# Performance work log

Measured on AMD Instinct MI355X. Metric: run time of the kernel, lower is better.

Reference implementation:

```python
import jax, jax.numpy as jnp
import numpy as np

D_MODEL = 256
N_LAYERS = 8
NUM_CLASSES = 3
INPUT_DIM = 1
BATCH = 8
SEQ = 2048
EXIT_IDX = (1, 3, 5, 7)  # n_layers//4-1, n_layers//2-1, 3n//4-1, n-1
LN_EPS = 1e-5


def setup_inputs() -> dict:
    key = jax.random.key(0)
    ks = jax.random.split(key, 16)
    d, nl, nc = D_MODEL, N_LAYERS, NUM_CLASSES
    return {
        "x": jax.random.normal(ks[0], (BATCH, SEQ, INPUT_DIM), jnp.float32),
        "in_W": jax.random.normal(ks[1], (d, INPUT_DIM), jnp.float32) * 0.02,
        "in_b": jnp.zeros((d,), jnp.float32),
        "A_params": jax.random.normal(ks[2], (nl, d), jnp.float32) * 0.1,
        "B_params": jax.random.normal(ks[3], (nl, d), jnp.float32),
        "C_params": jax.random.normal(ks[4], (nl, d), jnp.float32),
        "D_params": jax.random.normal(ks[5], (nl, d), jnp.float32),
        "proj_W": jax.random.normal(ks[6], (nl, d, d), jnp.float32) * 0.02,
        "proj_b": jnp.zeros((nl, d), jnp.float32),
        "ln_g": jnp.ones((nl, d), jnp.float32),
        "ln_b": jnp.zeros((nl, d), jnp.float32),
        "head_W": jax.random.normal(ks[7], (4, nc, d), jnp.float32) * 0.02,
        "head_b": jnp.zeros((4, nc), jnp.float32),
    }


def _ssm_block(x, Ap, Bp, Cp, Dp, pW, pb, g, b):
    # x: [B, L, d]
    Bsz, L, d = x.shape
    A = jax.nn.sigmoid(Ap)                               # [d]
    t = jnp.arange(L, dtype=jnp.float32)
    K = (Cp[:, None] * (A[:, None] ** t[None, :]) * Bp[:, None])[:, None, :]  # [d,1,L]
    xt = jnp.swapaxes(x, 1, 2)                           # [B, d, L]
    # torch F.conv1d(pad=L-1, groups=d) then [..., :L] == left-pad-only cross-correlation
    out = jax.lax.conv_general_dilated(
        xt, K, window_strides=(1,), padding=[(L - 1, 0)], feature_group_count=d
    )                                                    # [B, d, L]
    out = out + Dp[None, :, None] * xt
    out = jnp.swapaxes(out, 1, 2)                        # [B, L, d]
    out = jax.nn.gelu(out, approximate=False) @ pW.T + pb
    y = x + out
    mu = jnp.mean(y, axis=-1, keepdims=True)
    var = jnp.var(y, axis=-1, keepdims=True)
    return (y - mu) / jnp.sqrt(var + LN_EPS) * g + b


def reference(x, in_W, in_b, A_params, B_params, C_params, D_params,
              proj_W, proj_b, ln_g, ln_b, head_W, head_b):
    h = x @ in_W.T + in_b                                # [B, L, d]
    logits = []
    head = 0
    for i in range(N_LAYERS):
        h = _ssm_block(h, A_params[i], B_params[i], C_params[i], D_params[i],
                       proj_W[i], proj_b[i], ln_g[i], ln_b[i])
        if i in EXIT_IDX:
            pooled = jnp.mean(h, axis=1)                 # [B, d]
            logits.append(pooled @ head_W[head].T + head_b[head])
            head += 1
    return jnp.stack(logits, axis=0)                     # [4, B, num_classes]
```

## Files before the change

### kernel.cpp

```cpp
#include <hip/hip_runtime.h>
#include <math.h>

#define DM 256
#define LSEQ 2048
#define BATCH 8
#define NLAYER 8
#define EMAX 192
#define LN_EPS 1e-5f
#define BM 32
#define BLKS 64
#define NPROD 7
#define TAILB 57
#define ROWS (BATCH * LSEQ)

#define HT_STRIDE 1040
#define AB_OFF   33280
#define AL_OFF   (AB_OFF + 16384)
#define RED_OFF  (AL_OFF + 16384)
#define SMEM_SZ  (RED_OFF + 1280)

typedef float f32x4 __attribute__((ext_vector_type(4)));
typedef short bf16x8 __attribute__((ext_vector_type(8)));
typedef unsigned short u16;
typedef unsigned short u16x4 __attribute__((ext_vector_type(4)));
typedef unsigned short u16x8 __attribute__((ext_vector_type(8)));

union V8 { u16x8 u; bf16x8 b; };

__device__ __forceinline__ float erf_fast(float x) {
    float ax = fabsf(x);
    float t = __builtin_amdgcn_rcpf(fmaf(0.3275911f, ax, 1.f));
    float p = fmaf(t, 1.061405429f, -1.453152027f);
    p = fmaf(t, p, 1.421413741f);
    p = fmaf(t, p, -0.284496736f);
    p = fmaf(t, p, 0.254829592f);
    p = p * t;
    float e = __expf(-ax * ax);
    float r = 1.f - p * e;
    return copysignf(r, x);
}

__device__ __forceinline__ float gelu_fast(float v) {
    return 0.5f * v * (1.f + erf_fast(v * 0.70710678118654752f));
}

__device__ __forceinline__ void split2(float g, u16& hi, u16& lo) {
    unsigned u = __float_as_uint(g);
    hi = (u16)(u >> 16);
    float fh = __uint_as_float(u & 0xFFFF0000u);
    float r = g - fh;
    unsigned v = __float_as_uint(r);
    v = v + 0x7FFFu + ((v >> 16) & 1u);
    lo = (u16)(v >> 16);
}

__global__ void k_prepW(const float* __restrict__ pW, u16* __restrict__ pWh,
                        u16* __restrict__ pWl) {
    int i = blockIdx.x * blockDim.x + threadIdx.x;
    int e = i * 8;
    int l = e >> 16;
    int r = e & 65535;
    int cg = r >> 12;
    int ks = (r >> 9) & 7;
    int lane = (r >> 3) & 63;
    int fq = lane >> 4, fr = lane & 15;
    int col = (cg >> 2) * 64 + (cg & 3) * 16 + fr;
    int k = ks * 32 + fq * 8;
    const float* src = pW + l * 65536 + col * 256 + k;
    float4 w0 = *(const float4*)src;
    float4 w1 = *(const float4*)(src + 4);
    float vv[8] = {w0.x, w0.y, w0.z, w0.w, w1.x, w1.y, w1.z, w1.w};
    u16 sh[8], sl[8];
#pragma unroll
    for (int j = 0; j < 8; ++j) split2(vv[j], sh[j], sl[j]);
    u16x8 vh = {sh[0], sh[1], sh[2], sh[3], sh[4], sh[5], sh[6], sh[7]};
    u16x8 vl = {sl[0], sl[1], sl[2], sl[3], sl[4], sl[5], sl[6], sl[7]};
    *(u16x8*)&pWh[e] = vh;
    *(u16x8*)&pWl[e] = vl;
}

__global__ void k_prep0(const float* __restrict__ x, const float* __restrict__ inW,
                        const float* __restrict__ inb, const float* __restrict__ Ap,
                        const float* __restrict__ Bp, const float* __restrict__ Cp,
                        float* __restrict__ P_all, float* __restrict__ logA_all,
                        float* __restrict__ CB_all, float* __restrict__ pooled,
                        int* __restrict__ flags) {
    int b = blockIdx.x;
    int c = threadIdx.x;
    float A0 = 1.f / (1.f + expf(-Ap[c]));
    float iw = inW[c], ib = inb[c];
    const float* xb = x + b * LSEQ;
    float pw = 1.f, acc = 0.f;
    for (int t = 0; t <= EMAX; ++t) {
        acc += (xb[t] * iw + ib) * pw;
        pw *= A0;
    }
    P_all[b * DM + c] = acc;
    for (int l = 1; l < NLAYER; ++l) P_all[l * BATCH * DM + b * DM + c] = 0.f;
    for (int e = 0; e < 4; ++e) pooled[e * BATCH * DM + b * DM + c] = 0.f;
    if (b == 0) {
        for (int l = 0; l < NLAYER; ++l) {
            float Al = 1.f / (1.f + expf(-Ap[l * DM + c]));
            logA_all[l * DM + c] = logf(Al);
            CB_all[l * DM + c]   = Bp[l * DM + c] * Cp[l * DM + c];
        }
        if (c < NLAYER * BATCH) flags[c] = 0;
    }
}

__global__ __launch_bounds__(256, 2) void k_fused(
    const float* __restrict__ x, const float* __restrict__ inW,
    const float* __restrict__ inb,
    const u16* __restrict__ pWh, const u16* __restrict__ pWl,
    const float* __restrict__ Dp_all, const float* __restrict__ pb_all,
    const float* __restrict__ lng_all, const float* __restrict__ lnb_all,
    const float* __restrict__ logA_all, const float* __restrict__ CB_all,
    float* __restrict__ P_all, float* __restrict__ pooled,
    int* __restrict__ flags)
{
    __shared__ __align__(16) char smem[SMEM_SZ];

    int tid  = threadIdx.x;
    int lane = tid & 63;
    int wn   = tid >> 6;
    int fr   = lane & 15;
    int fq   = lane >> 4;

    int b    = blockIdx.x >> 6;
    int blk  = blockIdx.x & 63;
    int brow = b * LSEQ + blk * BM;
    bool isTail = (blk >= TAILB);
    bool isProd = (blk < NPROD);

    int srow = tid >> 3;
    int gr_s = brow + srow;
    int t_s  = gr_s & (LSEQ - 1);
    int u_s  = (LSEQ - 1) - t_s;
    bool tail_s = (u_s <= EMAX);
    float uf = (float)u_s;
    float xv = x[gr_s];

    float hreg[2][4][4];
    float* Pbuf = (float*)(smem + RED_OFF);

    for (int l = 0; l < NLAYER; ++l) {
        const float* Dp  = Dp_all   + l * DM;
        const float* la  = logA_all + l * DM;
        const float* cbp = CB_all   + l * DM;

        if (isTail) {
            if (l >= 1 && tid == 0) {
                while (__hip_atomic_load(&flags[l * BATCH + b], __ATOMIC_ACQUIRE,
                                         __HIP_MEMORY_SCOPE_AGENT) < NPROD)
                    __builtin_amdgcn_s_sleep(2);
            }
            __syncthreads();
            if (tid < DM)
                Pbuf[tid] = __hip_atomic_load(
                    &P_all[(size_t)l * BATCH * DM + b * DM + tid],
                    __ATOMIC_RELAXED, __HIP_MEMORY_SCOPE_AGENT);
            __syncthreads();
        }

        const u16* bhp = pWh + (size_t)l * 65536 + wn * 16384 + lane * 8;
        const u16* blp = pWl + (size_t)l * 65536 + wn * 16384 + lane * 8;
        V8 bhd[2][4], bld[2][4];
#pragma unroll
        for (int n = 0; n < 4; ++n) {
            bhd[0][n].u = *(const u16x8*)&bhp[n * 4096];
            bld[0][n].u = *(const u16x8*)&blp[n * 4096];
        }

#pragma unroll
        for (int i = 0; i < 4; ++i) {
            int u  = (tid & 7) + 8 * i;
            int kk = u * 8;
            int hby = srow * HT_STRIDE + u * 32;
            float hv[8];
            if (l == 0) {
                float4 w0 = *(const float4*)&inW[kk], w1 = *(const float4*)&inW[kk + 4];
                float4 b0 = *(const float4*)&inb[kk], b1 = *(const float4*)&inb[kk + 4];
                hv[0] = fmaf(xv, w0.x, b0.x); hv[1] = fmaf(xv, w0.y, b0.y);
                hv[2] = fmaf(xv, w0.z, b0.z); hv[3] = fmaf(xv, w0.w, b0.w);
                hv[4] = fmaf(xv, w1.x, b1.x); hv[5] = fmaf(xv, w1.y, b1.y);
                hv[6] = fmaf(xv, w1.z, b1.z); hv[7] = fmaf(xv, w1.w, b1.w);
                float4 o0 = {hv[0], hv[1], hv[2], hv[3]};
                float4 o1 = {hv[4], hv[5], hv[6], hv[7]};
                *(float4*)(smem + hby) = o0;
                *(float4*)(smem + hby + 16) = o1;
            } else {
                float4 h0 = *(const float4*)(smem + hby);
                float4 h1 = *(const float4*)(smem + hby + 16);
                hv[0] = h0.x; hv[1] = h0.y; hv[2] = h0.z; hv[3] = h0.w;
                hv[4] = h1.x; hv[5] = h1.y; hv[6] = h1.z; hv[7] = h1.w;
            }
            float4 d0 = *(const float4*)&Dp[kk];
            float4 d1 = *(const float4*)&Dp[kk + 4];
            float vv[8];
            vv[0] = hv[0] * d0.x; vv[1] = hv[1] * d0.y;
            vv[2] = hv[2] * d0.z; vv[3] = hv[3] * d0.w;
            vv[4] = hv[4] * d1.x; vv[5] = hv[5] * d1.y;
            vv[6] = hv[6] * d1.z; vv[7] = hv[7] * d1.w;
            if (tail_s) {
                float4 la0 = *(const float4*)&la[kk],  la1 = *(const float4*)&la[kk + 4];
                float4 cb0 = *(const float4*)&cbp[kk], cb1 = *(const float4*)&cbp[kk + 4];
                float4 P0  = *(const float4*)&Pbuf[kk], P1 = *(const float4*)&Pbuf[kk + 4];
                vv[0] += cb0.x * __expf(uf * la0.x) * P0.x;
                vv[1] += cb0.y * __expf(uf * la0.y) * P0.y;
                vv[2] += cb0.z * __expf(uf * la0.z) * P0.z;
                vv[3] += cb0.w * __expf(uf * la0.w) * P0.w;
                vv[4] += cb1.x * __expf(uf * la1.x) * P1.x;
                vv[5] += cb1.y * __expf(uf * la1.y) * P1.y;
                vv[6] += cb1.z * __expf(uf * la1.z) * P1.z;
                vv[7] += cb1.w * __expf(uf * la1.w) * P1.w;
            }
            u16 sh[8], sl[8];
#pragma unroll
            for (int j = 0; j < 8; ++j) split2(gelu_fast(vv[j]), sh[j], sl[j]);
            u16x8 vh = {sh[0], sh[1], sh[2], sh[3], sh[4], sh[5], sh[6], sh[7]};
            u16x8 vl = {sl[0], sl[1], sl[2], sl[3], sl[4], sl[5], sl[6], sl[7]};
            int aby = srow * 512 + ((u ^ (srow & 7)) << 4);
            *(u16x8*)(smem + AB_OFF + aby) = vh;
            *(u16x8*)(smem + AL_OFF + aby) = vl;
        }
        __syncthreads();

        f32x4 acc[2][4];
#pragma unroll
        for (int m = 0; m < 2; ++m)
#pragma unroll
            for (int n = 0; n < 4; ++n) acc[m][n] = (f32x4){0.f, 0.f, 0.f, 0.f};

#pragma unroll
        for (int ks = 0; ks < 8; ++ks) {
            int cur = ks & 1, nxt = cur ^ 1;
            if (ks < 7) {
#pragma unroll
                for (int n = 0; n < 4; ++n) {
                    bhd[nxt][n].u = *(const u16x8*)&bhp[n * 4096 + (ks + 1) * 512];
                    bld[nxt][n].u = *(const u16x8*)&blp[n * 4096 + (ks + 1) * 512];
                }
            }
            V8 ah[2], al[2];
#pragma unroll
            for (int m = 0; m < 2; ++m) {
                int row = m * 16 + fr;
                int aby = row * 512 + (((ks * 4 + fq) ^ (row & 7)) << 4);
                ah[m].u = *(const u16x8*)(smem + AB_OFF + aby);
                al[m].u = *(const u16x8*)(smem + AL_OFF + aby);
            }
#pragma unroll
            for (int m = 0; m < 2; ++m)
#pragma unroll
                for (int n = 0; n < 4; ++n) {
                    acc[m][n] = __builtin_amdgcn_mfma_f32_16x16x32_bf16(ah[m].b, bhd[cur][n].b, acc[m][n], 0, 0, 0);
                    acc[m][n] = __builtin_amdgcn_mfma_f32_16x16x32_bf16(ah[m].b, bld[cur][n].b, acc[m][n], 0, 0, 0);
                    acc[m][n] = __builtin_amdgcn_mfma_f32_16x16x32_bf16(al[m].b, bhd[cur][n].b, acc[m][n], 0, 0, 0);
                }
        }

        if (l == 0) {
#pragma unroll
            for (int m = 0; m < 2; ++m)
#pragma unroll
                for (int n = 0; n < 4; ++n)
#pragma unroll
                    for (int r = 0; r < 4; ++r) {
                        int row = m * 16 + fq * 4 + r;
                        int col = wn * 64 + n * 16 + fr;
                        hreg[m][n][r] = *(const float*)(smem + row * HT_STRIDE + col * 4);
                    }
        }
        float pbv[4], lgv[4], lbv[4];
#pragma unroll
        for (int n = 0; n < 4; ++n) {
            int col = wn * 64 + n * 16 + fr;
            pbv[n] = pb_all[l * DM + col];
            lgv[n] = lng_all[l * DM + col];
            lbv[n] = lnb_all[l * DM + col];
        }
        float s[2][4], ss[2][4];
#pragma unroll
        for (int m = 0; m < 2; ++m)
#pragma unroll
            for (int r = 0; r < 4; ++r) {
                float sy = 0.f, sy2 = 0.f;
#pragma unroll
                for (int n = 0; n < 4; ++n) {
                    float y = hreg[m][n][r] + acc[m][n][r] + pbv[n];
                    acc[m][n][r] = y;
                    sy += y; sy2 += y * y;
                }
                s[m][r] = sy; ss[m][r] = sy2;
            }
#pragma unroll
        for (int m = 0; m < 2; ++m)
#pragma unroll
            for (int r = 0; r < 4; ++r)
#pragma unroll
                for (int msk = 1; msk < 16; msk <<= 1) {
                    s[m][r]  += __shfl_xor(s[m][r],  msk);
                    ss[m][r] += __shfl_xor(ss[m][r], msk);
                }
        if (fr == 0) {
#pragma unroll
            for (int m = 0; m < 2; ++m)
#pragma unroll
                for (int r = 0; r < 4; ++r) {
                    int row = m * 16 + fq * 4 + r;
                    *(float*)(smem + RED_OFF + (row * 10 + wn * 2)     * 4) = s[m][r];
                    *(float*)(smem + RED_OFF + (row * 10 + wn * 2 + 1) * 4) = ss[m][r];
                }
        }
        __syncthreads();

        float mean[2][4], rstd[2][4];
#pragma unroll
        for (int m = 0; m < 2; ++m)
#pragma unroll
            for (int r = 0; r < 4; ++r) {
                int row = m * 16 + fq * 4 + r;
                float st = 0.f, sst = 0.f;
#pragma unroll
                for (int w = 0; w < 4; ++w) {
                    st  += *(const float*)(smem + RED_OFF + (row * 10 + w * 2)     * 4);
                    sst += *(const float*)(smem + RED_OFF + (row * 10 + w * 2 + 1) * 4);
                }
                float mu = st * (1.f / 256.f);
                float var = sst * (1.f / 256.f) - mu * mu;
                mean[m][r] = mu;
                rstd[m][r] = rsqrtf(var + LN_EPS);
            }
        int slot = (l == 1) ? 0 : (l == 3) ? 1 : (l == 5) ? 2 : (l == 7) ? 3 : -1;
        bool prod = (l < NLAYER - 1) && isProd;
        float lanv[4];
        if (prod) {
            const float* lan = logA_all + (l + 1) * DM;
#pragma unroll
            for (int n = 0; n < 4; ++n) lanv[n] = lan[wn * 64 + n * 16 + fr];
        }
        float cs[4] = {0.f, 0.f, 0.f, 0.f};
        float pc[4] = {0.f, 0.f, 0.f, 0.f};
#pragma unroll
        for (int m = 0; m < 2; ++m)
#pragma unroll
            for (int r = 0; r < 4; ++r) {
                int row  = m * 16 + fq * 4 + r;
                int trow = blk * BM + row;
#pragma unroll
                for (int n = 0; n < 4; ++n) {
                    float o = (acc[m][n][r] - mean[m][r]) * rstd[m][r] * lgv[n] + lbv[n];
                    hreg[m][n][r] = o;
                    int col = wn * 64 + n * 16 + fr;
                    *(float*)(smem + row * HT_STRIDE + col * 4) = o;
                    if (slot >= 0) cs[n] += o;
                    if (prod && trow <= EMAX) pc[n] += o * __expf((float)trow * lanv[n]);
                }
            }
        if (slot >= 0) {
#pragma unroll
            for (int n = 0; n < 4; ++n) {
                cs[n] += __shfl_xor(cs[n], 16);
                cs[n] += __shfl_xor(cs[n], 32);
            }
            if (lane < 16) {
#pragma unroll
                for (int n = 0; n < 4; ++n)
                    atomicAdd(&pooled[slot * (BATCH * DM) + b * DM + wn * 64 + n * 16 + lane], cs[n]);
            }
        }
        if (prod) {
#pragma unroll
            for (int n = 0; n < 4; ++n) {
                pc[n] += __shfl_xor(pc[n], 16);
                pc[n] += __shfl_xor(pc[n], 32);
            }
            if (lane < 16) {
#pragma unroll
                for (int n = 0; n < 4; ++n)
                    atomicAdd(&P_all[(size_t)(l + 1) * BATCH * DM + b * DM + wn * 64 + n * 16 + lane], pc[n]);
            }
        }
        __syncthreads();
        if (prod && tid == 0)
            __hip_atomic_fetch_add(&flags[(l + 1) * BATCH + b], 1,
                                   __ATOMIC_RELEASE, __HIP_MEMORY_SCOPE_AGENT);
    }
}

__global__ void k_head(const float* __restrict__ pooled, const float* __restrict__ hW,
                       const float* __restrict__ hb, float* __restrict__ out) {
    int tid = threadIdx.x;
    if (tid >= 96) return;
    int e = tid / 24;
    int r = tid % 24;
    int b = r / 3;
    int n = r % 3;
    const float* pv = &pooled[e * (BATCH * DM) + b * DM];
    const float* wv = &hW[(e * 3 + n) * DM];
    float acc = 0.f;
    for (int c = 0; c < DM; ++c) acc += pv[c] * wv[c];
    out[e * 24 + b * 3 + n] = acc * (1.f / (float)LSEQ) + hb[e * 3 + n];
}

extern "C" void kernel_launch(void* const* d_in, const int* in_sizes, int n_in,
                              void* d_out, int out_size, void* d_ws, size_t ws_size,
                              hipStream_t stream) {
    const float* x   = (const float*)d_in[0];
    const float* inW = (const float*)d_in[1];
    const float* inb = (const float*)d_in[2];
    const float* Ap  = (const float*)d_in[3];
    const float* Bp  = (const float*)d_in[4];
    const float* Cp  = (const float*)d_in[5];
    const float* Dp  = (const float*)d_in[6];
    const float* pW  = (const float*)d_in[7];
    const float* pb  = (const float*)d_in[8];
    const float* lng = (const float*)d_in[9];
    const float* lnb = (const float*)d_in[10];
    const float* hW  = (const float*)d_in[11];
    const float* hb  = (const float*)d_in[12];
    float* out = (float*)d_out;

    float* ws = (float*)d_ws;
    float* P_all    = ws;
    float* logA_all = P_all + NLAYER * BATCH * DM;
    float* CB_all   = logA_all + NLAYER * DM;
    float* pooled   = CB_all + NLAYER * DM;
    u16* pWh        = (u16*)(pooled + 4 * BATCH * DM);
    u16* pWl        = pWh + NLAYER * DM * DM;
    int* flags      = (int*)(pWl + NLAYER * DM * DM);

    k_prepW<<<(NLAYER * DM * DM / 8) / 256, 256, 0, stream>>>(pW, pWh, pWl);
    k_prep0<<<BATCH, 256, 0, stream>>>(x, inW, inb, Ap, Bp, Cp,
                                       P_all, logA_all, CB_all, pooled, flags);
    k_fused<<<BATCH * BLKS, 256, 0, stream>>>(
        x, inW, inb, pWh, pWl, Dp, pb, lng, lnb,
        logA_all, CB_all, P_all, pooled, flags);
    k_head<<<1, 128, 0, stream>>>(pooled, hW, hb, out);
}
```

Baseline: 121.7 us.

## Merge prep kernels, split A staging into halves, triple-buffer B prefetch

Merges the two prep kernels into one launch to cut launch overhead. Inside the fused kernel, the A-tile staging is split into two halves so MFMAs on the first half start before the second half is staged. B fragments move to a three-deep prefetch, with the next layer's first fragment loaded before the end-of-layer barrier. It also raises wave priority around the MFMA bursts and skips the smem store of the last layer's output. The cost is more registers for the extra B buffer, which could lower occupancy under launch_bounds(256,2).

```diff
diff --git a/kernel.cpp b/kernel.cpp
--- a/kernel.cpp
+++ b/kernel.cpp
@@ -11,7 +11,6 @@
 #define BLKS 64
 #define NPROD 7
 #define TAILB 57
-#define ROWS (BATCH * LSEQ)
 
 #define HT_STRIDE 1040
 #define AB_OFF   33280
@@ -22,7 +21,6 @@
 typedef float f32x4 __attribute__((ext_vector_type(4)));
 typedef short bf16x8 __attribute__((ext_vector_type(8)));
 typedef unsigned short u16;
-typedef unsigned short u16x4 __attribute__((ext_vector_type(4)));
 typedef unsigned short u16x8 __attribute__((ext_vector_type(8)));
 
 union V8 { u16x8 u; bf16x8 b; };
@@ -54,57 +52,58 @@
     lo = (u16)(v >> 16);
 }
 
-__global__ void k_prepW(const float* __restrict__ pW, u16* __restrict__ pWh,
-                        u16* __restrict__ pWl) {
-    int i = blockIdx.x * blockDim.x + threadIdx.x;
-    int e = i * 8;
-    int l = e >> 16;
-    int r = e & 65535;
-    int cg = r >> 12;
-    int ks = (r >> 9) & 7;
-    int lane = (r >> 3) & 63;
-    int fq = lane >> 4, fr = lane & 15;
-    int col = (cg >> 2) * 64 + (cg & 3) * 16 + fr;
-    int k = ks * 32 + fq * 8;
-    const float* src = pW + l * 65536 + col * 256 + k;
-    float4 w0 = *(const float4*)src;
-    float4 w1 = *(const float4*)(src + 4);
-    float vv[8] = {w0.x, w0.y, w0.z, w0.w, w1.x, w1.y, w1.z, w1.w};
-    u16 sh[8], sl[8];
-#pragma unroll
-    for (int j = 0; j < 8; ++j) split2(vv[j], sh[j], sl[j]);
-    u16x8 vh = {sh[0], sh[1], sh[2], sh[3], sh[4], sh[5], sh[6], sh[7]};
-    u16x8 vl = {sl[0], sl[1], sl[2], sl[3], sl[4], sl[5], sl[6], sl[7]};
-    *(u16x8*)&pWh[e] = vh;
-    *(u16x8*)&pWl[e] = vl;
-}
-
-__global__ void k_prep0(const float* __restrict__ x, const float* __restrict__ inW,
-                        const float* __restrict__ inb, const float* __restrict__ Ap,
-                        const float* __restrict__ Bp, const float* __restrict__ Cp,
-                        float* __restrict__ P_all, float* __restrict__ logA_all,
-                        float* __restrict__ CB_all, float* __restrict__ pooled,
-                        int* __restrict__ flags) {
-    int b = blockIdx.x;
-    int c = threadIdx.x;
-    float A0 = 1.f / (1.f + expf(-Ap[c]));
-    float iw = inW[c], ib = inb[c];
-    const float* xb = x + b * LSEQ;
-    float pw = 1.f, acc = 0.f;
-    for (int t = 0; t <= EMAX; ++t) {
-        acc += (xb[t] * iw + ib) * pw;
-        pw *= A0;
-    }
-    P_all[b * DM + c] = acc;
-    for (int l = 1; l < NLAYER; ++l) P_all[l * BATCH * DM + b * DM + c] = 0.f;
-    for (int e = 0; e < 4; ++e) pooled[e * BATCH * DM + b * DM + c] = 0.f;
-    if (b == 0) {
-        for (int l = 0; l < NLAYER; ++l) {
-            float Al = 1.f / (1.f + expf(-Ap[l * DM + c]));
-            logA_all[l * DM + c] = logf(Al);
-            CB_all[l * DM + c]   = Bp[l * DM + c] * Cp[l * DM + c];
-        }
-        if (c < NLAYER * BATCH) flags[c] = 0;
+__global__ void k_prep(const float* __restrict__ pW, u16* __restrict__ pWh,
+                       u16* __restrict__ pWl,
+                       const float* __restrict__ x, const float* __restrict__ inW,
+                       const float* __restrict__ inb, const float* __restrict__ Ap,
+                       const float* __restrict__ Bp, const float* __restrict__ Cp,
+                       float* __restrict__ P_all, float* __restrict__ logA_all,
+                       float* __restrict__ CB_all, float* __restrict__ pooled,
+                       int* __restrict__ flags) {
+    if (blockIdx.x < 256) {
+        int i = blockIdx.x * 256 + threadIdx.x;
+        int e = i * 8;
+        int l = e >> 16;
+        int r = e & 65535;
+        int cg = r >> 12;
+        int ks = (r >> 9) & 7;
+        int lane = (r >> 3) & 63;
+        int fq = lane >> 4, fr = lane & 15;
+        int col = (cg >> 2) * 64 + (cg & 3) * 16 + fr;
+        int k = ks * 32 + fq * 8;
+        const float* src = pW + l * 65536 + col * 256 + k;
+        float4 w0 = *(const float4*)src;
+        float4 w1 = *(const float4*)(src + 4);
+        float vv[8] = {w0.x, w0.y, w0.z, w0.w, w1.x, w1.y, w1.z, w1.w};
+        u16 sh[8], sl[8];
+#pragma unroll
+        for (int j = 0; j < 8; ++j) split2(vv[j], sh[j], sl[j]);
+        u16x8 vh = {sh[0], sh[1], sh[2], sh[3], sh[4], sh[5], sh[6], sh[7]};
+        u16x8 vl = {sl[0], sl[1], sl[2], sl[3], sl[4], sl[5], sl[6], sl[7]};
+        *(u16x8*)&pWh[e] = vh;
+        *(u16x8*)&pWl[e] = vl;
+    } else {
+        int b = blockIdx.x - 256;
+        int c = threadIdx.x;
+        float A0 = 1.f / (1.f + expf(-Ap[c]));
+        float iw = inW[c], ib = inb[c];
+        const float* xb = x + b * LSEQ;
+        float pw = 1.f, acc = 0.f;
+        for (int t = 0; t <= EMAX; ++t) {
+            acc += (xb[t] * iw + ib) * pw;
+            pw *= A0;
+        }
+        P_all[b * DM + c] = acc;
+        for (int l = 1; l < NLAYER; ++l) P_all[l * BATCH * DM + b * DM + c] = 0.f;
+        for (int e = 0; e < 4; ++e) pooled[e * BATCH * DM + b * DM + c] = 0.f;
+        if (b == 0) {
+            for (int l = 0; l < NLAYER; ++l) {
+                float Al = 1.f / (1.f + expf(-Ap[l * DM + c]));
+                logA_all[l * DM + c] = logf(Al);
+                CB_all[l * DM + c]   = Bp[l * DM + c] * Cp[l * DM + c];
+            }
+            if (c < NLAYER * BATCH) flags[c] = 0;
+        }
     }
 }
 
@@ -143,36 +142,10 @@
     float hreg[2][4][4];
     float* Pbuf = (float*)(smem + RED_OFF);
 
-    for (int l = 0; l < NLAYER; ++l) {
-        const float* Dp  = Dp_all   + l * DM;
-        const float* la  = logA_all + l * DM;
-        const float* cbp = CB_all   + l * DM;
-
-        if (isTail) {
-            if (l >= 1 && tid == 0) {
-                while (__hip_atomic_load(&flags[l * BATCH + b], __ATOMIC_ACQUIRE,
-                                         __HIP_MEMORY_SCOPE_AGENT) < NPROD)
-                    __builtin_amdgcn_s_sleep(2);
-            }
-            __syncthreads();
-            if (tid < DM)
-                Pbuf[tid] = __hip_atomic_load(
-                    &P_all[(size_t)l * BATCH * DM + b * DM + tid],
-                    __ATOMIC_RELAXED, __HIP_MEMORY_SCOPE_AGENT);
-            __syncthreads();
-        }
-
-        const u16* bhp = pWh + (size_t)l * 65536 + wn * 16384 + lane * 8;
-        const u16* blp = pWl + (size_t)l * 65536 + wn * 16384 + lane * 8;
-        V8 bhd[2][4], bld[2][4];
-#pragma unroll
-        for (int n = 0; n < 4; ++n) {
-            bhd[0][n].u = *(const u16x8*)&bhp[n * 4096];
-            bld[0][n].u = *(const u16x8*)&blp[n * 4096];
-        }
-
-#pragma unroll
-        for (int i = 0; i < 4; ++i) {
+    auto stage_half = [&](int l, int i0, int i1,
+                          const float* Dp, const float* la, const float* cbp) {
+#pragma unroll
+        for (int i = i0; i < i1; ++i) {
             int u  = (tid & 7) + 8 * i;
             int kk = u * 8;
             int hby = srow * HT_STRIDE + u * 32;
@@ -223,6 +196,41 @@
             *(u16x8*)(smem + AB_OFF + aby) = vh;
             *(u16x8*)(smem + AL_OFF + aby) = vl;
         }
+    };
+
+    V8 bhd[3][4], bld[3][4];
+    {
+        const u16* bhp0 = pWh + wn * 16384 + lane * 8;
+        const u16* blp0 = pWl + wn * 16384 + lane * 8;
+#pragma unroll
+        for (int n = 0; n < 4; ++n) {
+            bhd[0][n].u = *(const u16x8*)&bhp0[n * 4096];
+            bld[0][n].u = *(const u16x8*)&blp0[n * 4096];
+        }
+    }
+
+    for (int l = 0; l < NLAYER; ++l) {
+        const float* Dp  = Dp_all   + l * DM;
+        const float* la  = logA_all + l * DM;
+        const float* cbp = CB_all   + l * DM;
+        const u16* bhp = pWh + (size_t)l * 65536 + wn * 16384 + lane * 8;
+        const u16* blp = pWl + (size_t)l * 65536 + wn * 16384 + lane * 8;
+
+        if (isTail) {
+            if (l >= 1 && tid == 0) {
+                while (__hip_atomic_load(&flags[l * BATCH + b], __ATOMIC_ACQUIRE,
+                                         __HIP_MEMORY_SCOPE_AGENT) < NPROD)
+                    __builtin_amdgcn_s_sleep(2);
+            }
+            __syncthreads();
+            if (tid < DM)
+                Pbuf[tid] = __hip_atomic_load(
+                    &P_all[(size_t)l * BATCH * DM + b * DM + tid],
+                    __ATOMIC_RELAXED, __HIP_MEMORY_SCOPE_AGENT);
+            __syncthreads();
+        }
+
+        stage_half(l, 0, 2, Dp, la, cbp);
         __syncthreads();
 
         f32x4 acc[2][4];
@@ -232,14 +240,19 @@
             for (int n = 0; n < 4; ++n) acc[m][n] = (f32x4){0.f, 0.f, 0.f, 0.f};
 
 #pragma unroll
-        for (int ks = 0; ks < 8; ++ks) {
-            int cur = ks & 1, nxt = cur ^ 1;
-            if (ks < 7) {
-#pragma unroll
-                for (int n = 0; n < 4; ++n) {
-                    bhd[nxt][n].u = *(const u16x8*)&bhp[n * 4096 + (ks + 1) * 512];
-                    bld[nxt][n].u = *(const u16x8*)&blp[n * 4096 + (ks + 1) * 512];
-                }
+        for (int n = 0; n < 4; ++n) {
+            bhd[1][n].u = *(const u16x8*)&bhp[n * 4096 + 512];
+            bld[1][n].u = *(const u16x8*)&blp[n * 4096 + 512];
+        }
+
+#pragma unroll
+        for (int ks = 0; ks < 4; ++ks) {
+            int cur = ks % 3;
+            int pf  = (ks + 2) % 3;
+#pragma unroll
+            for (int n = 0; n < 4; ++n) {
+                bhd[pf][n].u = *(const u16x8*)&bhp[n * 4096 + (ks + 2) * 512];
+                bld[pf][n].u = *(const u16x8*)&blp[n * 4096 + (ks + 2) * 512];
             }
             V8 ah[2], al[2];
 #pragma unroll
@@ -249,6 +262,7 @@
                 ah[m].u = *(const u16x8*)(smem + AB_OFF + aby);
                 al[m].u = *(const u16x8*)(smem + AL_OFF + aby);
             }
+            __builtin_amdgcn_s_setprio(1);
 #pragma unroll
             for (int m = 0; m < 2; ++m)
 #pragma unroll
@@ -257,8 +271,53 @@
                     acc[m][n] = __builtin_amdgcn_mfma_f32_16x16x32_bf16(ah[m].b, bld[cur][n].b, acc[m][n], 0, 0, 0);
                     acc[m][n] = __builtin_amdgcn_mfma_f32_16x16x32_bf16(al[m].b, bhd[cur][n].b, acc[m][n], 0, 0, 0);
                 }
-        }
-
+            __builtin_amdgcn_s_setprio(0);
+        }
+
+        stage_half(l, 2, 4, Dp, la, cbp);
+        __syncthreads();
+
+#pragma unroll
+        for (int ks = 4; ks < 8; ++ks) {
+            int cur = ks % 3;
+            if (ks < 6) {
+                int pf = (ks + 2) % 3;
+#pragma unroll
+                for (int n = 0; n < 4; ++n) {
+                    bhd[pf][n].u = *(const u16x8*)&bhp[n * 4096 + (ks + 2) * 512];
+                    bld[pf][n].u = *(const u16x8*)&blp[n * 4096 + (ks + 2) * 512];
+                }
+            }
+            V8 ah[2], al[2];
+#pragma unroll
+            for (int m = 0; m < 2; ++m) {
+                int row = m * 16 + fr;
+                int aby = row * 512 + (((ks * 4 + fq) ^ (row & 7)) << 4);
+                ah[m].u = *(const u16x8*)(smem + AB_OFF + aby);
+                al[m].u = *(const u16x8*)(smem + AL_OFF + aby);
+            }
+            __builtin_amdgcn_s_setprio(1);
+#pragma unroll
+            for (int m = 0; m < 2; ++m)
+#pragma unroll
+                for (int n = 0; n < 4; ++n) {
+                    acc[m][n] = __builtin_amdgcn_mfma_f32_16x16x32_bf16(ah[m].b, bhd[cur][n].b, acc[m][n], 0, 0, 0);
+                    acc[m][n] = __builtin_amdgcn_mfma_f32_16x16x32_bf16(ah[m].b, bld[cur][n].b, acc[m][n], 0, 0, 0);
+                    acc[m][n] = __builtin_amdgcn_mfma_f32_16x16x32_bf16(al[m].b, bhd[cur][n].b, acc[m][n], 0, 0, 0);
+                }
+            __builtin_amdgcn_s_setprio(0);
+        }
+
+        int cols[4];
+#pragma unroll
+        for (int n = 0; n < 4; ++n) cols[n] = wn * 64 + n * 16 + fr;
+        float pbv[4], lgv[4], lbv[4];
+#pragma unroll
+        for (int n = 0; n < 4; ++n) {
+            pbv[n] = pb_all[l * DM + cols[n]];
+            lgv[n] = lng_all[l * DM + cols[n]];
+            lbv[n] = lnb_all[l * DM + cols[n]];
+        }
         if (l == 0) {
 #pragma unroll
             for (int m = 0; m < 2; ++m)
@@ -267,17 +326,8 @@
 #pragma unroll
                     for (int r = 0; r < 4; ++r) {
                         int row = m * 16 + fq * 4 + r;
-                        int col = wn * 64 + n * 16 + fr;
-                        hreg[m][n][r] = *(const float*)(smem + row * HT_STRIDE + col * 4);
+                        hreg[m][n][r] = *(const float*)(smem + row * HT_STRIDE + cols[n] * 4);
                     }
-        }
-        float pbv[4], lgv[4], lbv[4];
-#pragma unroll
-        for (int n = 0; n < 4; ++n) {
-            int col = wn * 64 + n * 16 + fr;
-            pbv[n] = pb_all[l * DM + col];
-            lgv[n] = lng_all[l * DM + col];
-            lbv[n] = lnb_all[l * DM + col];
         }
         float s[2][4], ss[2][4];
 #pragma unroll
@@ -332,12 +382,12 @@
                 rstd[m][r] = rsqrtf(var + LN_EPS);
             }
         int slot = (l == 1) ? 0 : (l == 3) ? 1 : (l == 5) ? 2 : (l == 7) ? 3 : -1;
-        bool prod = (l < NLAYER - 1) && isProd;
+        bool last = (l == NLAYER - 1);
+        bool prod = !last && isProd;
         float lanv[4];
         if (prod) {
-            const float* lan = logA_all + (l + 1) * DM;
-#pragma unroll
-            for (int n = 0; n < 4; ++n) lanv[n] = lan[wn * 64 + n * 16 + fr];
+#pragma unroll
+            for (int n = 0; n < 4; ++n) lanv[n] = logA_all[(l + 1) * DM + cols[n]];
         }
         float cs[4] = {0.f, 0.f, 0.f, 0.f};
         float pc[4] = {0.f, 0.f, 0.f, 0.f};
@@ -351,8 +401,7 @@
                 for (int n = 0; n < 4; ++n) {
                     float o = (acc[m][n][r] - mean[m][r]) * rstd[m][r] * lgv[n] + lbv[n];
                     hreg[m][n][r] = o;
-                    int col = wn * 64 + n * 16 + fr;
-                    *(float*)(smem + row * HT_STRIDE + col * 4) = o;
+                    if (!last) *(float*)(smem + row * HT_STRIDE + cols[n] * 4) = o;
                     if (slot >= 0) cs[n] += o;
                     if (prod && trow <= EMAX) pc[n] += o * __expf((float)trow * lanv[n]);
                 }
@@ -381,10 +430,20 @@
                     atomicAdd(&P_all[(size_t)(l + 1) * BATCH * DM + b * DM + wn * 64 + n * 16 + lane], pc[n]);
             }
         }
-        __syncthreads();
-        if (prod && tid == 0)
-            __hip_atomic_fetch_add(&flags[(l + 1) * BATCH + b], 1,
-                                   __ATOMIC_RELEASE, __HIP_MEMORY_SCOPE_AGENT);
+
+        if (!last) {
+            const u16* bhpN = pWh + (size_t)(l + 1) * 65536 + wn * 16384 + lane * 8;
+            const u16* blpN = pWl + (size_t)(l + 1) * 65536 + wn * 16384 + lane * 8;
+#pragma unroll
+            for (int n = 0; n < 4; ++n) {
+                bhd[0][n].u = *(const u16x8*)&bhpN[n * 4096];
+                bld[0][n].u = *(const u16x8*)&blpN[n * 4096];
+            }
+            __syncthreads();
+            if (prod && tid == 0)
+                __hip_atomic_fetch_add(&flags[(l + 1) * BATCH + b], 1,
+                                       __ATOMIC_RELEASE, __HIP_MEMORY_SCOPE_AGENT);
+        }
     }
 }
 
@@ -430,9 +489,8 @@
     u16* pWl        = pWh + NLAYER * DM * DM;
     int* flags      = (int*)(pWl + NLAYER * DM * DM);
 
-    k_prepW<<<(NLAYER * DM * DM / 8) / 256, 256, 0, stream>>>(pW, pWh, pWl);
-    k_prep0<<<BATCH, 256, 0, stream>>>(x, inW, inb, Ap, Bp, Cp,
-                                       P_all, logA_all, CB_all, pooled, flags);
+    k_prep<<<264, 256, 0, stream>>>(pW, pWh, pWl, x, inW, inb, Ap, Bp, Cp,
+                                    P_all, logA_all, CB_all, pooled, flags);
     k_fused<<<BATCH * BLKS, 256, 0, stream>>>(
         x, inW, inb, pWh, pWl, Dp, pb, lng, lnb,
         logA_all, CB_all, P_all, pooled, flags);
```

New measurement: 153.6 us. 26.2% more time.

## Merge prep kernels, add MFMA priority, stagger half the blocks, skip last-layer stores

Applied to the files above, without the earlier changes.

Fuses the weight-split and per-batch prep kernels into one launch to remove one kernel launch and its gap. Raises wave priority around the MFMA burst with s_setprio. Inserts s_sleep delays for blocks with bit 256 set to stagger start times. Hoists the per-column parameter loads before the l==0 readback and skips the shared-memory h store on the last layer. The sleep adds latency for half the blocks, and it may or may not pay off through reduced contention.

```diff
diff --git a/kernel.cpp b/kernel.cpp
--- a/kernel.cpp
+++ b/kernel.cpp
@@ -11,7 +11,6 @@
 #define BLKS 64
 #define NPROD 7
 #define TAILB 57
-#define ROWS (BATCH * LSEQ)
 
 #define HT_STRIDE 1040
 #define AB_OFF   33280
@@ -22,7 +21,6 @@
 typedef float f32x4 __attribute__((ext_vector_type(4)));
 typedef short bf16x8 __attribute__((ext_vector_type(8)));
 typedef unsigned short u16;
-typedef unsigned short u16x4 __attribute__((ext_vector_type(4)));
 typedef unsigned short u16x8 __attribute__((ext_vector_type(8)));
 
 union V8 { u16x8 u; bf16x8 b; };
@@ -54,57 +52,58 @@
     lo = (u16)(v >> 16);
 }
 
-__global__ void k_prepW(const float* __restrict__ pW, u16* __restrict__ pWh,
-                        u16* __restrict__ pWl) {
-    int i = blockIdx.x * blockDim.x + threadIdx.x;
-    int e = i * 8;
-    int l = e >> 16;
-    int r = e & 65535;
-    int cg = r >> 12;
-    int ks = (r >> 9) & 7;
-    int lane = (r >> 3) & 63;
-    int fq = lane >> 4, fr = lane & 15;
-    int col = (cg >> 2) * 64 + (cg & 3) * 16 + fr;
-    int k = ks * 32 + fq * 8;
-    const float* src = pW + l * 65536 + col * 256 + k;
-    float4 w0 = *(const float4*)src;
-    float4 w1 = *(const float4*)(src + 4);
-    float vv[8] = {w0.x, w0.y, w0.z, w0.w, w1.x, w1.y, w1.z, w1.w};
-    u16 sh[8], sl[8];
-#pragma unroll
-    for (int j = 0; j < 8; ++j) split2(vv[j], sh[j], sl[j]);
-    u16x8 vh = {sh[0], sh[1], sh[2], sh[3], sh[4], sh[5], sh[6], sh[7]};
-    u16x8 vl = {sl[0], sl[1], sl[2], sl[3], sl[4], sl[5], sl[6], sl[7]};
-    *(u16x8*)&pWh[e] = vh;
-    *(u16x8*)&pWl[e] = vl;
-}
-
-__global__ void k_prep0(const float* __restrict__ x, const float* __restrict__ inW,
-                        const float* __restrict__ inb, const float* __restrict__ Ap,
-                        const float* __restrict__ Bp, const float* __restrict__ Cp,
-                        float* __restrict__ P_all, float* __restrict__ logA_all,
-                        float* __restrict__ CB_all, float* __restrict__ pooled,
-                        int* __restrict__ flags) {
-    int b = blockIdx.x;
-    int c = threadIdx.x;
-    float A0 = 1.f / (1.f + expf(-Ap[c]));
-    float iw = inW[c], ib = inb[c];
-    const float* xb = x + b * LSEQ;
-    float pw = 1.f, acc = 0.f;
-    for (int t = 0; t <= EMAX; ++t) {
-        acc += (xb[t] * iw + ib) * pw;
-        pw *= A0;
-    }
-    P_all[b * DM + c] = acc;
-    for (int l = 1; l < NLAYER; ++l) P_all[l * BATCH * DM + b * DM + c] = 0.f;
-    for (int e = 0; e < 4; ++e) pooled[e * BATCH * DM + b * DM + c] = 0.f;
-    if (b == 0) {
-        for (int l = 0; l < NLAYER; ++l) {
-            float Al = 1.f / (1.f + expf(-Ap[l * DM + c]));
-            logA_all[l * DM + c] = logf(Al);
-            CB_all[l * DM + c]   = Bp[l * DM + c] * Cp[l * DM + c];
-        }
-        if (c < NLAYER * BATCH) flags[c] = 0;
+__global__ void k_prep(const float* __restrict__ pW, u16* __restrict__ pWh,
+                       u16* __restrict__ pWl,
+                       const float* __restrict__ x, const float* __restrict__ inW,
+                       const float* __restrict__ inb, const float* __restrict__ Ap,
+                       const float* __restrict__ Bp, const float* __restrict__ Cp,
+                       float* __restrict__ P_all, float* __restrict__ logA_all,
+                       float* __restrict__ CB_all, float* __restrict__ pooled,
+                       int* __restrict__ flags) {
+    if (blockIdx.x < 256) {
+        int i = blockIdx.x * 256 + threadIdx.x;
+        int e = i * 8;
+        int l = e >> 16;
+        int r = e & 65535;
+        int cg = r >> 12;
+        int ks = (r >> 9) & 7;
+        int lane = (r >> 3) & 63;
+        int fq = lane >> 4, fr = lane & 15;
+        int col = (cg >> 2) * 64 + (cg & 3) * 16 + fr;
+        int k = ks * 32 + fq * 8;
+        const float* src = pW + l * 65536 + col * 256 + k;
+        float4 w0 = *(const float4*)src;
+        float4 w1 = *(const float4*)(src + 4);
+        float vv[8] = {w0.x, w0.y, w0.z, w0.w, w1.x, w1.y, w1.z, w1.w};
+        u16 sh[8], sl[8];
+#pragma unroll
+        for (int j = 0; j < 8; ++j) split2(vv[j], sh[j], sl[j]);
+        u16x8 vh = {sh[0], sh[1], sh[2], sh[3], sh[4], sh[5], sh[6], sh[7]};
+        u16x8 vl = {sl[0], sl[1], sl[2], sl[3], sl[4], sl[5], sl[6], sl[7]};
+        *(u16x8*)&pWh[e] = vh;
+        *(u16x8*)&pWl[e] = vl;
+    } else {
+        int b = blockIdx.x - 256;
+        int c = threadIdx.x;
+        float A0 = 1.f / (1.f + expf(-Ap[c]));
+        float iw = inW[c], ib = inb[c];
+        const float* xb = x + b * LSEQ;
+        float pw = 1.f, acc = 0.f;
+        for (int t = 0; t <= EMAX; ++t) {
+            acc += (xb[t] * iw + ib) * pw;
+            pw *= A0;
+        }
+        P_all[b * DM + c] = acc;
+        for (int l = 1; l < NLAYER; ++l) P_all[l * BATCH * DM + b * DM + c] = 0.f;
+        for (int e = 0; e < 4; ++e) pooled[e * BATCH * DM + b * DM + c] = 0.f;
+        if (b == 0) {
+            for (int l = 0; l < NLAYER; ++l) {
+                float Al = 1.f / (1.f + expf(-Ap[l * DM + c]));
+                logA_all[l * DM + c] = logf(Al);
+                CB_all[l * DM + c]   = Bp[l * DM + c] * Cp[l * DM + c];
+            }
+            if (c < NLAYER * BATCH) flags[c] = 0;
+        }
     }
 }
 
@@ -131,6 +130,11 @@
     int brow = b * LSEQ + blk * BM;
     bool isTail = (blk >= TAILB);
     bool isProd = (blk < NPROD);
+
+    if (blockIdx.x & 256) {
+        __builtin_amdgcn_s_sleep(127);
+        __builtin_amdgcn_s_sleep(127);
+    }
 
     int srow = tid >> 3;
     int gr_s = brow + srow;
@@ -249,6 +253,7 @@
                 ah[m].u = *(const u16x8*)(smem + AB_OFF + aby);
                 al[m].u = *(const u16x8*)(smem + AL_OFF + aby);
             }
+            __builtin_amdgcn_s_setprio(1);
 #pragma unroll
             for (int m = 0; m < 2; ++m)
 #pragma unroll
@@ -257,8 +262,19 @@
                     acc[m][n] = __builtin_amdgcn_mfma_f32_16x16x32_bf16(ah[m].b, bld[cur][n].b, acc[m][n], 0, 0, 0);
                     acc[m][n] = __builtin_amdgcn_mfma_f32_16x16x32_bf16(al[m].b, bhd[cur][n].b, acc[m][n], 0, 0, 0);
                 }
-        }
-
+            __builtin_amdgcn_s_setprio(0);
+        }
+
+        int cols[4];
+#pragma unroll
+        for (int n = 0; n < 4; ++n) cols[n] = wn * 64 + n * 16 + fr;
+        float pbv[4], lgv[4], lbv[4];
+#pragma unroll
+        for (int n = 0; n < 4; ++n) {
+            pbv[n] = pb_all[l * DM + cols[n]];
+            lgv[n] = lng_all[l * DM + cols[n]];
+            lbv[n] = lnb_all[l * DM + cols[n]];
+        }
         if (l == 0) {
 #pragma unroll
             for (int m = 0; m < 2; ++m)
@@ -267,17 +283,8 @@
 #pragma unroll
                     for (int r = 0; r < 4; ++r) {
                         int row = m * 16 + fq * 4 + r;
-                        int col = wn * 64 + n * 16 + fr;
-                        hreg[m][n][r] = *(const float*)(smem + row * HT_STRIDE + col * 4);
+                        hreg[m][n][r] = *(const float*)(smem + row * HT_STRIDE + cols[n] * 4);
                     }
-        }
-        float pbv[4], lgv[4], lbv[4];
-#pragma unroll
-        for (int n = 0; n < 4; ++n) {
-            int col = wn * 64 + n * 16 + fr;
-            pbv[n] = pb_all[l * DM + col];
-            lgv[n] = lng_all[l * DM + col];
-            lbv[n] = lnb_all[l * DM + col];
         }
         float s[2][4], ss[2][4];
 #pragma unroll
@@ -332,12 +339,12 @@
                 rstd[m][r] = rsqrtf(var + LN_EPS);
             }
         int slot = (l == 1) ? 0 : (l == 3) ? 1 : (l == 5) ? 2 : (l == 7) ? 3 : -1;
-        bool prod = (l < NLAYER - 1) && isProd;
+        bool last = (l == NLAYER - 1);
+        bool prod = !last && isProd;
         float lanv[4];
         if (prod) {
-            const float* lan = logA_all + (l + 1) * DM;
-#pragma unroll
-            for (int n = 0; n < 4; ++n) lanv[n] = lan[wn * 64 + n * 16 + fr];
+#pragma unroll
+            for (int n = 0; n < 4; ++n) lanv[n] = logA_all[(l + 1) * DM + cols[n]];
         }
         float cs[4] = {0.f, 0.f, 0.f, 0.f};
         float pc[4] = {0.f, 0.f, 0.f, 0.f};
@@ -351,8 +358,7 @@
                 for (int n = 0; n < 4; ++n) {
                     float o = (acc[m][n][r] - mean[m][r]) * rstd[m][r] * lgv[n] + lbv[n];
                     hreg[m][n][r] = o;
-                    int col = wn * 64 + n * 16 + fr;
-                    *(float*)(smem + row * HT_STRIDE + col * 4) = o;
+                    if (!last) *(float*)(smem + row * HT_STRIDE + cols[n] * 4) = o;
                     if (slot >= 0) cs[n] += o;
                     if (prod && trow <= EMAX) pc[n] += o * __expf((float)trow * lanv[n]);
                 }
@@ -430,9 +436,8 @@
     u16* pWl        = pWh + NLAYER * DM * DM;
     int* flags      = (int*)(pWl + NLAYER * DM * DM);
 
-    k_prepW<<<(NLAYER * DM * DM / 8) / 256, 256, 0, stream>>>(pW, pWh, pWl);
-    k_prep0<<<BATCH, 256, 0, stream>>>(x, inW, inb, Ap, Bp, Cp,
-                                       P_all, logA_all, CB_all, pooled, flags);
+    k_prep<<<264, 256, 0, stream>>>(pW, pWh, pWl, x, inW, inb, Ap, Bp, Cp,
+                                    P_all, logA_all, CB_all, pooled, flags);
     k_fused<<<BATCH * BLKS, 256, 0, stream>>>(
         x, inW, inb, pWh, pWl, Dp, pb, lng, lnb,
         logA_all, CB_all, P_all, pooled, flags);
```

Result: no change. 122.3 us (+0.5%).
